# Kernel tuning notes

Measured on AMD Instinct MI355X. Metric: run time of the kernel, lower is better.

The kernel has to match this reference:

```python
import jax, jax.numpy as jnp
import numpy as np


def setup_inputs() -> dict:
    key = jax.random.key(0)
    ks = jax.random.split(key, 6)
    B, H, F, X, T = 8, 32, 8, 128, 256
    z0 = jax.random.normal(ks[0], (B, H, X), jnp.float32)
    xi = jax.random.normal(ks[1], (B, F, X, T), jnp.float32)
    A = jax.random.normal(ks[2], (H, H), jnp.float32) * 0.1
    Gw = jax.random.normal(ks[3], (H, F, H), jnp.float32) * 0.1
    Wr = jax.random.normal(ks[4], (X, H, H, H), jnp.float32) * 1e-4
    Wi = jax.random.normal(ks[5], (X, H, H, H), jnp.float32) * 1e-4
    return {"z0": z0, "xi": xi, "A": A, "Gw": Gw, "Wr": Wr, "Wi": Wi}


def reference(z0, xi, A, Gw, Wr, Wi):
    # z0: (B, H, X); xi: (B, F, X, T)
    B, Hc, X = z0.shape
    T = xi.shape[-1]

    # Initial guess u(t) = z0 for all t (reconstruction of the fixed-point seed).
    u = jnp.broadcast_to(z0[..., None], (B, Hc, X, T))

    # Linear SPDE right-hand side: Fu = A u, Gu = Gw u.
    Fu = jnp.einsum('ih,bhxt->bixt', A, u)
    Gu = jnp.einsum('ifh,bhxt->bifxt', Gw, u)          # (B, H, F, X, T)
    Guxi = jnpum = None
    Guxi = jnp.einsum('bifxt,bfxt->bixt', Gu, xi)
    Hu = Fu + Guxi                                      # (B, H, X, T)

    # Spatial FFT (axis 2) + fftshift, as in the torch module.
    H_ft = jnp.fft.fftshift(jnp.fft.fft(Hu, axis=2), axes=2)    # complex64
    z0_ft = jnp.fft.fftshift(jnp.fft.fft(z0, axis=2), axes=2)   # (B, H, X)

    # Per-Fourier-mode complex-linear CDE vector field weights.
    W = (Wr + 1j * Wi).astype(jnp.complex64)            # (X, H, H, H)

    # Control path X(t): (B, X, T, H); Euler increments at the knots.
    Hp = jnp.transpose(H_ft, (0, 2, 3, 1))
    dX = Hp[:, :, 1:, :] - Hp[:, :, :-1, :]             # (B, X, T-1, H)
    z_init = jnp.transpose(z0_ft, (0, 2, 1))            # (B, X, H)

    def step(z, dx):
        # f(z)[b, x, i, c] = sum_j W[x, i, c, j] z[b, x, j]
        fz = jnp.einsum('xicj,bxj->bxic', W, z)
        z_new = z + jnp.einsum('bxic,bxc->bxi', fz, dx)  # dz = f(z) . dX
        return z_new, z_new

    _, zs = jax.lax.scan(step, z_init, jnp.moveaxis(dX, 2, 0))
    zs = jnp.concatenate([z_init[None], zs], axis=0)    # (T, B, X, H)
    z_all = jnp.transpose(zs, (1, 3, 2, 0))             # (B, H, X, T)

    u_new = jnp.fft.ifft(jnp.fft.ifftshift(z_all, axes=2), axis=2)
    return u_new.real
```

## Files before the change

kernel.cpp:

```cpp
#include <hip/hip_runtime.h>
#include <math.h>

#define Bc 8
#define Hc 32
#define Fc 8
#define Xc 128
#define Tc 256

typedef __bf16 bf16x8 __attribute__((ext_vector_type(8)));
typedef float f32x4 __attribute__((ext_vector_type(4)));

__device__ __forceinline__ int bitrev7(int x) { return (int)(__brev((unsigned)x) >> 25); }

__device__ __forceinline__ unsigned pack_bf16(float a, float b) {
    unsigned ua = __float_as_uint(a);
    unsigned ub = __float_as_uint(b);
    ua = (ua + 0x7FFFu + ((ua >> 16) & 1u)) >> 16;
    ub = (ub + 0x7FFFu + ((ub >> 16) & 1u)) & 0xFFFF0000u;
    return (ua & 0xFFFFu) | ub;
}
__device__ __forceinline__ float bf16_val(float a) {
    unsigned ua = __float_as_uint(a);
    ua = (ua + 0x7FFFu + ((ua >> 16) & 1u)) & 0xFFFF0000u;
    return __uint_as_float(ua);
}

__device__ __forceinline__ void bfly(float2& a, float2& b, float2 twv, float sign) {
    float cs = twv.x, sn = sign * twv.y;
    float2 bw = make_float2(cs * b.x - sn * b.y, cs * b.y + sn * b.x);
    float2 na = make_float2(a.x + bw.x, a.y + bw.y);
    b = make_float2(a.x - bw.x, a.y - bw.y);
    a = na;
}

#define FRS 129
template <int NTHR>
__device__ __forceinline__ void fft32x128(float2* buf, float sign) {
    __shared__ float2 tw[128];
    int tid = threadIdx.x;
    if (tid >= 1 && tid < 128) {
        int h = 1 << (31 - __builtin_clz((unsigned)tid));
        int pos = tid - h;
        float sn, cs;
        __sincosf(3.14159265358979f * (float)pos / (float)h, &sn, &cs);
        tw[tid] = make_float2(cs, sn);
    }
    __syncthreads();
    for (int grp = tid; grp < 32 * 16; grp += NTHR) {
        float2* p = buf + (grp >> 4) * FRS + (grp & 15) * 8;
        float2 v[8];
#pragma unroll
        for (int e = 0; e < 8; ++e) v[e] = p[e];
        bfly(v[0], v[1], tw[1], sign); bfly(v[2], v[3], tw[1], sign);
        bfly(v[4], v[5], tw[1], sign); bfly(v[6], v[7], tw[1], sign);
        bfly(v[0], v[2], tw[2], sign); bfly(v[1], v[3], tw[3], sign);
        bfly(v[4], v[6], tw[2], sign); bfly(v[5], v[7], tw[3], sign);
        bfly(v[0], v[4], tw[4], sign); bfly(v[1], v[5], tw[5], sign);
        bfly(v[2], v[6], tw[6], sign); bfly(v[3], v[7], tw[7], sign);
#pragma unroll
        for (int e = 0; e < 8; ++e) p[e] = v[e];
    }
    __syncthreads();
    for (int grp = tid; grp < 32 * 32; grp += NTHR) {
        int row = grp >> 5, sub = grp & 31;
        int m = sub & 7, k = sub >> 3;
        float2* p = buf + row * FRS + k * 32 + m;
        float2 v0 = p[0], v1 = p[8], v2 = p[16], v3 = p[24];
        bfly(v0, v1, tw[8 + m], sign);
        bfly(v2, v3, tw[8 + m], sign);
        bfly(v0, v2, tw[16 + m], sign);
        bfly(v1, v3, tw[16 + m + 8], sign);
        p[0] = v0; p[8] = v1; p[16] = v2; p[24] = v3;
    }
    __syncthreads();
    for (int grp = tid; grp < 32 * 32; grp += NTHR) {
        int row = grp >> 5, m2 = grp & 31;
        float2* p = buf + row * FRS + m2;
        float2 v0 = p[0], v1 = p[32], v2 = p[64], v3 = p[96];
        bfly(v0, v1, tw[32 + m2], sign);
        bfly(v2, v3, tw[32 + m2], sign);
        bfly(v0, v2, tw[64 + m2], sign);
        bfly(v1, v3, tw[64 + m2 + 32], sign);
        p[0] = v0; p[32] = v1; p[64] = v2; p[96] = v3;
    }
    __syncthreads();
}

__global__ void k_xit(const float* __restrict__ xi, float* __restrict__ xiT) {
    __shared__ float tile[32][33];
    int bid = blockIdx.x;
    int bf = bid >> 3, tt = bid & 7;
    int t0 = tt * 32;
    int tid = threadIdx.x;
    for (int xt = 0; xt < 4; ++xt) {
        int x0 = xt * 32;
        __syncthreads();
        for (int idx = tid; idx < 1024; idx += 256) {
            int xr = idx >> 5, tc = idx & 31;
            tile[xr][tc] = xi[((size_t)bf * Xc + x0 + xr) * Tc + t0 + tc];
        }
        __syncthreads();
        for (int idx = tid; idx < 1024; idx += 256) {
            int tr = idx >> 5, xc = idx & 31;
            xiT[((size_t)bf * Tc + t0 + tr) * Xc + x0 + xc] = tile[xc][tr];
        }
    }
}

__global__ void k_pre(const float* __restrict__ z0, const float* __restrict__ A,
                      const float* __restrict__ Gw, float* __restrict__ Fz,
                      float* __restrict__ Gz, float2* __restrict__ Z0ft) {
    __shared__ float z0l[Hc * Xc];
    __shared__ float2 cbuf[Hc * FRS];
    int b = blockIdx.x;
    int tid = threadIdx.x;
    for (int idx = tid; idx < Hc * Xc; idx += 256) z0l[idx] = z0[b * Hc * Xc + idx];
    __syncthreads();
    for (int idx = tid; idx < Hc * Xc; idx += 256) {
        int i = idx >> 7, x = idx & 127;
        float s = 0.f;
        for (int h = 0; h < Hc; ++h) s += A[i * Hc + h] * z0l[h * 128 + x];
        Fz[b * Hc * Xc + idx] = s;
    }
    for (int idx = tid; idx < Hc * Fc * Xc; idx += 256) {
        int i = idx >> 10, f = (idx >> 7) & 7, x = idx & 127;
        float s = 0.f;
        for (int h = 0; h < Hc; ++h) s += Gw[(i * Fc + f) * Hc + h] * z0l[h * 128 + x];
        Gz[b * Hc * Fc * Xc + idx] = s;
    }
    for (int idx = tid; idx < Hc * Xc; idx += 256) {
        int h = idx >> 7, x = idx & 127;
        cbuf[h * FRS + bitrev7(x)] = make_float2(z0l[h * 128 + x], 0.f);
    }
    fft32x128<256>(cbuf, -1.f);
    for (int idx = tid; idx < Xc * Hc; idx += 256) {
        int xs = idx >> 5, h = idx & 31;
        Z0ft[(b * Xc + xs) * Hc + h] = cbuf[h * FRS + ((xs + 64) & 127)];
    }
}

__global__ void k_spec(const float* __restrict__ xiT, const float* __restrict__ Fz,
                       const float* __restrict__ Gz, float2* __restrict__ Hft) {
    __shared__ float xil[Fc * Xc];
    __shared__ float2 cbuf[Hc * FRS];
    int bid = blockIdx.x;
    int b = bid >> 8, t = bid & 255;
    int tid = threadIdx.x;
    for (int idx = tid; idx < Fc * Xc / 4; idx += 512) {
        int f = idx >> 5, xq = (idx & 31) * 4;
        *(float4*)(xil + f * 128 + xq) =
            *(const float4*)(xiT + ((size_t)(b * Fc + f) * Tc + t) * Xc + xq);
    }
    __syncthreads();
    for (int idx = tid; idx < Hc * Xc / 4; idx += 512) {
        int i = idx >> 5, xq = (idx & 31) * 4;
        float4 hu = *(const float4*)(Fz + b * Hc * Xc + i * 128 + xq);
        const float* gzp = Gz + (b * Hc + i) * (Fc * Xc) + xq;
#pragma unroll
        for (int f = 0; f < Fc; ++f) {
            float4 gz = *(const float4*)(gzp + f * 128);
            float4 xv = *(const float4*)(&xil[f * 128 + xq]);
            hu.x += gz.x * xv.x; hu.y += gz.y * xv.y;
            hu.z += gz.z * xv.z; hu.w += gz.w * xv.w;
        }
        cbuf[i * FRS + bitrev7(xq + 0)] = make_float2(hu.x, 0.f);
        cbuf[i * FRS + bitrev7(xq + 1)] = make_float2(hu.y, 0.f);
        cbuf[i * FRS + bitrev7(xq + 2)] = make_float2(hu.z, 0.f);
        cbuf[i * FRS + bitrev7(xq + 3)] = make_float2(hu.w, 0.f);
    }
    fft32x128<512>(cbuf, -1.f);
    for (int idx = tid; idx < Xc * Hc; idx += 512) {
        int xs = idx >> 5, i = idx & 31;
        Hft[((long)(b * Xc + xs) * Tc + t) * Hc + i] = cbuf[i * FRS + ((xs + 64) & 127)];
    }
}

#define ML_DW 16448
#define B_DW  1152
#define SCAN_LDS 150016

__device__ __forceinline__ void build_B(unsigned* Bb, int w, int tt, int c,
                                        float2 hp, float2 hn, float sc) {
    float dre = (hn.x - hp.x) * sc;
    float dim = (hn.y - hp.y) * sc;
    float hre = bf16_val(dre), hmim = bf16_val(-dim), him = bf16_val(dim);
    int n0 = w * 4 + tt * 2;
    Bb[n0 * 36 + c] = pack_bf16(hre, hmim);
    Bb[(n0 + 1) * 36 + c] = pack_bf16(him, hre);
    Bb[576 + n0 * 36 + c] = pack_bf16(dre - hre, (-dim) - hmim);
    Bb[576 + (n0 + 1) * 36 + c] = pack_bf16(dim - him, dre - hre);
}

__global__ __launch_bounds__(768, 3) void k_scan(const float* __restrict__ Wr,
                                                 const float* __restrict__ Wi,
                                                 const float2* __restrict__ Hft,
                                                 const float2* __restrict__ Z0ft,
                                                 float2* __restrict__ Zall) {
    extern __shared__ unsigned char smem[];
    float* Mlf = (float*)smem;
    unsigned* Aw = (unsigned*)smem;
    unsigned* Bd = (unsigned*)(smem + 131584);
    float* zlf = (float*)(smem + 140800);
    float2* zstc = (float2*)(smem + 141824);

    int tid = threadIdx.x;
    int x = blockIdx.x >> 1, g = blockIdx.x & 1;
    int lane = tid & 63, wid = tid >> 6;
    int isProd = (wid < 8);
    int p = wid;
    int w = isProd ? (wid & 3) : (wid - 8);
    int b = g * 4 + w;

    const float* wrp = Wr + (size_t)x * 32768;
    const float* wip = Wi + (size_t)x * 32768;
    for (int idx = tid; idx < 32768; idx += 768) {
        int j = idx & 31, cc = (idx >> 5) & 31, ii = idx >> 10;
        int r = ii * 32 + j;
        int pd = r * 32 + (((cc >> 2) ^ (r & 7)) << 2) + (cc & 3);
        Aw[pd] = pack_bf16(wrp[(ii * 32 + cc) * 32 + j], wip[(ii * 32 + cc) * 32 + j]);
    }
    __syncthreads();

    size_t bx = (size_t)(b * Xc + x);
    const float2* Hrow = Hft + bx * (Tc * Hc);
    float2* Zrow = Zall + bx * (Hc * Tc);
    int jq = lane >> 5, il = lane & 31;

    uint4 af[8][2];
    float2 Hp2 = make_float2(0.f, 0.f), Hn2 = make_float2(0.f, 0.f);
    float2 zr = make_float2(0.f, 0.f);

    if (isProd) {
        int n16 = lane & 15, q = lane >> 4;
        int rbase = p * 128 + n16;
#pragma unroll
        for (int mt = 0; mt < 8; ++mt) {
            int r = rbase + mt * 16;
#pragma unroll
            for (int kf = 0; kf < 2; ++kf) {
                int cg = (kf * 4 + q) ^ (r & 7);
                af[mt][kf] = *(const uint4*)(Aw + r * 32 + cg * 4);
            }
        }
    } else {
        __builtin_amdgcn_s_setprio(1);
        zr = Z0ft[bx * Hc + il];
        if (jq == 0) {
            ((float2*)(zlf + w * 64))[il] = zr;
            zstc[w * 256 + il] = zr;
        }
        float2 ha = Hrow[jq * 32 + il];
        float2 hb = Hrow[(1 + jq) * 32 + il];
        build_B(Bd, w, jq, il, ha, hb, 1.f);
        Hp2 = Hrow[(2 + jq) * 32 + il];
        Hn2 = Hrow[(3 + jq) * 32 + il];
    }
    __syncthreads();

#pragma unroll 1
    for (int k = 0; k <= 128; ++k) {
        if (isProd) {
            if (k < 128) {
                int bk = k & 1;
                int n = lane & 15, q = lane >> 4;
                const unsigned* Bb = Bd + bk * B_DW;
                bf16x8 bh0 = __builtin_bit_cast(bf16x8, *(const uint4*)(Bb + n * 36 + q * 4));
                bf16x8 bh1 = __builtin_bit_cast(bf16x8, *(const uint4*)(Bb + n * 36 + 16 + q * 4));
                bf16x8 bl0 = __builtin_bit_cast(bf16x8, *(const uint4*)(Bb + 576 + n * 36 + q * 4));
                bf16x8 bl1 = __builtin_bit_cast(bf16x8, *(const uint4*)(Bb + 576 + n * 36 + 16 + q * 4));
                float* Mb = Mlf + bk * ML_DW;
#pragma unroll
                for (int mt = 0; mt < 8; ++mt) {
                    f32x4 acc = {0.f, 0.f, 0.f, 0.f};
                    acc = __builtin_amdgcn_mfma_f32_16x16x32_bf16(
                        __builtin_bit_cast(bf16x8, af[mt][0]), bh0, acc, 0, 0, 0);
                    acc = __builtin_amdgcn_mfma_f32_16x16x32_bf16(
                        __builtin_bit_cast(bf16x8, af[mt][1]), bh1, acc, 0, 0, 0);
                    acc = __builtin_amdgcn_mfma_f32_16x16x32_bf16(
                        __builtin_bit_cast(bf16x8, af[mt][0]), bl0, acc, 0, 0, 0);
                    acc = __builtin_amdgcn_mfma_f32_16x16x32_bf16(
                        __builtin_bit_cast(bf16x8, af[mt][1]), bl1, acc, 0, 0, 0);
                    int i = p * 4 + (mt >> 1);
                    int jgp = ((((mt & 1) * 4) + q) ^ (i & 7)) ^ ((i >> 3) & 3);
                    *(f32x4*)(Mb + n * 1028 + i * 32 + jgp * 4) = acc;
                }
            }
        } else {
            float2 HpN = Hp2, HnN = Hn2;
            if (k + 2 <= 127) {
                int kc2 = k + 2;
                HpN = Hrow[(2 * kc2 + jq) * 32 + il];
                int t2 = 2 * kc2 + 1 + jq;
                if (t2 > 255) t2 = 255;
                HnN = Hrow[t2 * 32 + il];
            }
            if (k > 0) {
                int kc = k - 1;
                int bk = kc & 1;
#pragma unroll
                for (int s = 0; s < 2; ++s) {
                    int t = 2 * kc + 1 + s;
                    if (t > 255) break;
                    const float* base = Mlf + bk * ML_DW + (w * 4 + s * 2) * 1028 + il * 32;
                    float4 mr[4], mi[4];
#pragma unroll
                    for (int gg = 0; gg < 4; ++gg) {
                        int jg = (((jq * 4 + gg) ^ (il & 7) ^ ((il >> 3) & 3)) << 2);
                        mr[gg] = *(const float4*)(base + jg);
                        mi[gg] = *(const float4*)(base + 1028 + jg);
                    }
                    const float4* zf4 = (const float4*)(zlf + w * 64);
                    float yR = 0.f, yI = 0.f;
#pragma unroll
                    for (int gg = 0; gg < 4; ++gg) {
                        float4 za = zf4[jq * 8 + gg * 2];
                        float4 zb = zf4[jq * 8 + gg * 2 + 1];
                        yR += mr[gg].x * za.x - mi[gg].x * za.y + mr[gg].y * za.z - mi[gg].y * za.w
                            + mr[gg].z * zb.x - mi[gg].z * zb.y + mr[gg].w * zb.z - mi[gg].w * zb.w;
                        yI += mr[gg].x * za.y + mi[gg].x * za.x + mr[gg].y * za.w + mi[gg].y * za.z
                            + mr[gg].z * zb.y + mi[gg].z * zb.x + mr[gg].w * zb.w + mi[gg].w * zb.z;
                    }
                    yR += __shfl_xor(yR, 32);
                    yI += __shfl_xor(yI, 32);
                    zr.x += yR;
                    zr.y += yI;
                    if (jq == 0) {
                        ((float2*)(zlf + w * 64))[il] = zr;
                        zstc[w * 256 + (t & 7) * 32 + il] = zr;
                    }
                    if ((t & 7) == 7) {
                        int t0 = t - 7;
                        int i2 = lane >> 1, tb = (lane & 1) * 4;
                        float2 v0 = zstc[w * 256 + (tb + 0) * 32 + i2];
                        float2 v1 = zstc[w * 256 + (tb + 1) * 32 + i2];
                        float2 v2 = zstc[w * 256 + (tb + 2) * 32 + i2];
                        float2 v3 = zstc[w * 256 + (tb + 3) * 32 + i2];
                        *(float4*)(Zrow + i2 * Tc + t0 + tb) = make_float4(v0.x, v0.y, v1.x, v1.y);
                        *(float4*)(Zrow + i2 * Tc + t0 + tb + 2) = make_float4(v2.x, v2.y, v3.x, v3.y);
                    }
                }
            }
            if (k < 127) {
                float sc = (2 * (k + 1) + 1 + jq <= 255) ? 1.f : 0.f;
                build_B(Bd + ((k + 1) & 1) * B_DW, w, jq, il, Hp2, Hn2, sc);
                Hp2 = HpN;
                Hn2 = HnN;
            }
        }
        __syncthreads();
    }
}

__global__ void k_post(const float2* __restrict__ Zall, float* __restrict__ out) {
    __shared__ float2 cbuf[32 * FRS];
    int bid = blockIdx.x;
    int b = bid >> 8, i = (bid >> 3) & 31, tq = bid & 7;
    int t0 = tq * 32;
    int tid = threadIdx.x;
    for (int idx = tid; idx < 128 * 16; idx += 512) {
        int k = idx >> 4, tc2 = (idx & 15) * 2;
        int xg = (k + 64) & 127;
        float4 v = *(const float4*)(Zall + ((long)(b * Xc + xg) * Hc + i) * Tc + t0 + tc2);
        int kb = bitrev7(k);
        cbuf[tc2 * FRS + kb] = make_float2(v.x, v.y);
        cbuf[(tc2 + 1) * FRS + kb] = make_float2(v.z, v.w);
    }
    fft32x128<512>(cbuf, +1.f);
    const float inv = 1.0f / 128.0f;
    for (int idx = tid; idx < 128 * 32; idx += 512) {
        int xs = idx >> 5, tc = idx & 31;
        out[((long)(b * Hc + i) * Xc + xs) * Tc + t0 + tc] = cbuf[tc * FRS + xs].x * inv;
    }
}

extern "C" void kernel_launch(void* const* d_in, const int* in_sizes, int n_in,
                              void* d_out, int out_size, void* d_ws, size_t ws_size,
                              hipStream_t stream) {
    const float* z0 = (const float*)d_in[0];
    const float* xi = (const float*)d_in[1];
    const float* A = (const float*)d_in[2];
    const float* Gw = (const float*)d_in[3];
    const float* Wr = (const float*)d_in[4];
    const float* Wi = (const float*)d_in[5];
    float* out = (float*)d_out;
    char* ws = (char*)d_ws;

    float2* Hft = (float2*)(ws);
    float2* Zall = (float2*)(ws + 67108864);
    float2* Z0ft = (float2*)(ws + 134217728);
    float* Fz = (float*)(ws + 134479872);
    float* Gz = (float*)(ws + 134610944);
    float* xiT = (float*)(ws + 67108864);

    (void)hipFuncSetAttribute((const void*)k_scan,
                              hipFuncAttributeMaxDynamicSharedMemorySize, SCAN_LDS);

    k_xit<<<Bc * Fc * 8, 256, 0, stream>>>(xi, xiT);
    k_pre<<<Bc, 256, 0, stream>>>(z0, A, Gw, Fz, Gz, Z0ft);
    k_spec<<<Bc * Tc, 512, 0, stream>>>(xiT, Fz, Gz, Hft);
    k_scan<<<Xc * 2, 768, SCAN_LDS, stream>>>(Wr, Wi, Hft, Z0ft, Zall);
    k_post<<<Bc * Hc * 8, 512, 0, stream>>>(Zall, out);
}
```

Measured before the change: 414.2 us.

## Fuse final FFT stage into output writes and pad shared FFT layout

```diff
diff --git a/kernel.cpp b/kernel.cpp
--- a/kernel.cpp
+++ b/kernel.cpp
@@ -33,30 +33,35 @@
     a = na;
 }
 
-#define FRS 129
-template <int NTHR>
-__device__ __forceinline__ void fft32x128(float2* buf, float sign) {
-    __shared__ float2 tw[128];
-    int tid = threadIdx.x;
+#define RS 144
+__device__ __forceinline__ int AIX(int e) { return e + (e >> 3); }
+__device__ __forceinline__ int TWA(int t) { return (t >> 4) * RS + (t & 15) * 9 + 8; }
+
+__device__ __forceinline__ void fft_tw_init(float2* c, int tid) {
     if (tid >= 1 && tid < 128) {
         int h = 1 << (31 - __builtin_clz((unsigned)tid));
         int pos = tid - h;
         float sn, cs;
         __sincosf(3.14159265358979f * (float)pos / (float)h, &sn, &cs);
-        tw[tid] = make_float2(cs, sn);
-    }
-    __syncthreads();
+        c[TWA(tid)] = make_float2(cs, sn);
+    }
+}
+
+template <int NTHR>
+__device__ __forceinline__ void fft_ph12(float2* c, float sign, int tid) {
+    float2 t1 = c[TWA(1)], t2 = c[TWA(2)], t3 = c[TWA(3)];
+    float2 t4 = c[TWA(4)], t5 = c[TWA(5)], t6 = c[TWA(6)], t7 = c[TWA(7)];
     for (int grp = tid; grp < 32 * 16; grp += NTHR) {
-        float2* p = buf + (grp >> 4) * FRS + (grp & 15) * 8;
+        float2* p = c + (grp >> 4) * RS + (grp & 15) * 9;
         float2 v[8];
 #pragma unroll
         for (int e = 0; e < 8; ++e) v[e] = p[e];
-        bfly(v[0], v[1], tw[1], sign); bfly(v[2], v[3], tw[1], sign);
-        bfly(v[4], v[5], tw[1], sign); bfly(v[6], v[7], tw[1], sign);
-        bfly(v[0], v[2], tw[2], sign); bfly(v[1], v[3], tw[3], sign);
-        bfly(v[4], v[6], tw[2], sign); bfly(v[5], v[7], tw[3], sign);
-        bfly(v[0], v[4], tw[4], sign); bfly(v[1], v[5], tw[5], sign);
-        bfly(v[2], v[6], tw[6], sign); bfly(v[3], v[7], tw[7], sign);
+        bfly(v[0], v[1], t1, sign); bfly(v[2], v[3], t1, sign);
+        bfly(v[4], v[5], t1, sign); bfly(v[6], v[7], t1, sign);
+        bfly(v[0], v[2], t2, sign); bfly(v[1], v[3], t3, sign);
+        bfly(v[4], v[6], t2, sign); bfly(v[5], v[7], t3, sign);
+        bfly(v[0], v[4], t4, sign); bfly(v[1], v[5], t5, sign);
+        bfly(v[2], v[6], t6, sign); bfly(v[3], v[7], t7, sign);
 #pragma unroll
         for (int e = 0; e < 8; ++e) p[e] = v[e];
     }
@@ -64,26 +69,15 @@
     for (int grp = tid; grp < 32 * 32; grp += NTHR) {
         int row = grp >> 5, sub = grp & 31;
         int m = sub & 7, k = sub >> 3;
-        float2* p = buf + row * FRS + k * 32 + m;
-        float2 v0 = p[0], v1 = p[8], v2 = p[16], v3 = p[24];
-        bfly(v0, v1, tw[8 + m], sign);
-        bfly(v2, v3, tw[8 + m], sign);
-        bfly(v0, v2, tw[16 + m], sign);
-        bfly(v1, v3, tw[16 + m + 8], sign);
-        p[0] = v0; p[8] = v1; p[16] = v2; p[24] = v3;
-    }
-    __syncthreads();
-    for (int grp = tid; grp < 32 * 32; grp += NTHR) {
-        int row = grp >> 5, m2 = grp & 31;
-        float2* p = buf + row * FRS + m2;
-        float2 v0 = p[0], v1 = p[32], v2 = p[64], v3 = p[96];
-        bfly(v0, v1, tw[32 + m2], sign);
-        bfly(v2, v3, tw[32 + m2], sign);
-        bfly(v0, v2, tw[64 + m2], sign);
-        bfly(v1, v3, tw[64 + m2 + 32], sign);
-        p[0] = v0; p[32] = v1; p[64] = v2; p[96] = v3;
-    }
-    __syncthreads();
+        float2* p = c + row * RS + 36 * k + m;
+        float2 v0 = p[0], v1 = p[9], v2 = p[18], v3 = p[27];
+        float2 ta = c[TWA(8 + m)], tb = c[TWA(16 + m)], tc_ = c[TWA(24 + m)];
+        bfly(v0, v1, ta, sign);
+        bfly(v2, v3, ta, sign);
+        bfly(v0, v2, tb, sign);
+        bfly(v1, v3, tc_, sign);
+        p[0] = v0; p[9] = v1; p[18] = v2; p[27] = v3;
+    }
 }
 
 __global__ void k_xit(const float* __restrict__ xi, float* __restrict__ xiT) {
@@ -111,10 +105,11 @@
                       const float* __restrict__ Gw, float* __restrict__ Fz,
                       float* __restrict__ Gz, float2* __restrict__ Z0ft) {
     __shared__ float z0l[Hc * Xc];
-    __shared__ float2 cbuf[Hc * FRS];
+    __shared__ float2 cbuf[Hc * RS];
     int b = blockIdx.x;
     int tid = threadIdx.x;
     for (int idx = tid; idx < Hc * Xc; idx += 256) z0l[idx] = z0[b * Hc * Xc + idx];
+    fft_tw_init(cbuf, tid);
     __syncthreads();
     for (int idx = tid; idx < Hc * Xc; idx += 256) {
         int i = idx >> 7, x = idx & 127;
@@ -130,19 +125,31 @@
     }
     for (int idx = tid; idx < Hc * Xc; idx += 256) {
         int h = idx >> 7, x = idx & 127;
-        cbuf[h * FRS + bitrev7(x)] = make_float2(z0l[h * 128 + x], 0.f);
-    }
-    fft32x128<256>(cbuf, -1.f);
-    for (int idx = tid; idx < Xc * Hc; idx += 256) {
-        int xs = idx >> 5, h = idx & 31;
-        Z0ft[(b * Xc + xs) * Hc + h] = cbuf[h * FRS + ((xs + 64) & 127)];
+        cbuf[h * RS + AIX(bitrev7(x))] = make_float2(z0l[h * 128 + x], 0.f);
+    }
+    __syncthreads();
+    fft_ph12<256>(cbuf, -1.f, tid);
+    __syncthreads();
+    for (int grp = tid; grp < 1024; grp += 256) {
+        int h = grp & 31, m2 = grp >> 5;
+        float2* p = cbuf + h * RS + AIX(m2);
+        float2 v0 = p[0], v1 = p[36], v2 = p[72], v3 = p[108];
+        float2 ta = cbuf[TWA(32 + m2)], tb = cbuf[TWA(64 + m2)], tc_ = cbuf[TWA(96 + m2)];
+        bfly(v0, v1, ta, -1.f);
+        bfly(v2, v3, ta, -1.f);
+        bfly(v0, v2, tb, -1.f);
+        bfly(v1, v3, tc_, -1.f);
+        Z0ft[(b * Xc + m2 + 64) * Hc + h] = v0;
+        Z0ft[(b * Xc + m2 + 96) * Hc + h] = v1;
+        Z0ft[(b * Xc + m2) * Hc + h] = v2;
+        Z0ft[(b * Xc + m2 + 32) * Hc + h] = v3;
     }
 }
 
 __global__ void k_spec(const float* __restrict__ xiT, const float* __restrict__ Fz,
                        const float* __restrict__ Gz, float2* __restrict__ Hft) {
     __shared__ float xil[Fc * Xc];
-    __shared__ float2 cbuf[Hc * FRS];
+    __shared__ float2 cbuf[Hc * RS];
     int bid = blockIdx.x;
     int b = bid >> 8, t = bid & 255;
     int tid = threadIdx.x;
@@ -151,6 +158,7 @@
         *(float4*)(xil + f * 128 + xq) =
             *(const float4*)(xiT + ((size_t)(b * Fc + f) * Tc + t) * Xc + xq);
     }
+    fft_tw_init(cbuf, tid);
     __syncthreads();
     for (int idx = tid; idx < Hc * Xc / 4; idx += 512) {
         int i = idx >> 5, xq = (idx & 31) * 4;
@@ -163,15 +171,27 @@
             hu.x += gz.x * xv.x; hu.y += gz.y * xv.y;
             hu.z += gz.z * xv.z; hu.w += gz.w * xv.w;
         }
-        cbuf[i * FRS + bitrev7(xq + 0)] = make_float2(hu.x, 0.f);
-        cbuf[i * FRS + bitrev7(xq + 1)] = make_float2(hu.y, 0.f);
-        cbuf[i * FRS + bitrev7(xq + 2)] = make_float2(hu.z, 0.f);
-        cbuf[i * FRS + bitrev7(xq + 3)] = make_float2(hu.w, 0.f);
-    }
-    fft32x128<512>(cbuf, -1.f);
-    for (int idx = tid; idx < Xc * Hc; idx += 512) {
-        int xs = idx >> 5, i = idx & 31;
-        Hft[((long)(b * Xc + xs) * Tc + t) * Hc + i] = cbuf[i * FRS + ((xs + 64) & 127)];
+        cbuf[i * RS + AIX(bitrev7(xq + 0))] = make_float2(hu.x, 0.f);
+        cbuf[i * RS + AIX(bitrev7(xq + 1))] = make_float2(hu.y, 0.f);
+        cbuf[i * RS + AIX(bitrev7(xq + 2))] = make_float2(hu.z, 0.f);
+        cbuf[i * RS + AIX(bitrev7(xq + 3))] = make_float2(hu.w, 0.f);
+    }
+    __syncthreads();
+    fft_ph12<512>(cbuf, -1.f, tid);
+    __syncthreads();
+    for (int grp = tid; grp < 1024; grp += 512) {
+        int i = grp & 31, m2 = grp >> 5;
+        float2* p = cbuf + i * RS + AIX(m2);
+        float2 v0 = p[0], v1 = p[36], v2 = p[72], v3 = p[108];
+        float2 ta = cbuf[TWA(32 + m2)], tb = cbuf[TWA(64 + m2)], tc_ = cbuf[TWA(96 + m2)];
+        bfly(v0, v1, ta, -1.f);
+        bfly(v2, v3, ta, -1.f);
+        bfly(v0, v2, tb, -1.f);
+        bfly(v1, v3, tc_, -1.f);
+        Hft[((long)(b * Xc + m2 + 64) * Tc + t) * Hc + i] = v0;
+        Hft[((long)(b * Xc + m2 + 96) * Tc + t) * Hc + i] = v1;
+        Hft[((long)(b * Xc + m2) * Tc + t) * Hc + i] = v2;
+        Hft[((long)(b * Xc + m2 + 32) * Tc + t) * Hc + i] = v3;
     }
 }
 
@@ -352,7 +372,7 @@
 }
 
 __global__ void k_post(const float2* __restrict__ Zall, float* __restrict__ out) {
-    __shared__ float2 cbuf[32 * FRS];
+    __shared__ float2 cbuf[32 * RS];
     int bid = blockIdx.x;
     int b = bid >> 8, i = (bid >> 3) & 31, tq = bid & 7;
     int t0 = tq * 32;
@@ -361,15 +381,29 @@
         int k = idx >> 4, tc2 = (idx & 15) * 2;
         int xg = (k + 64) & 127;
         float4 v = *(const float4*)(Zall + ((long)(b * Xc + xg) * Hc + i) * Tc + t0 + tc2);
-        int kb = bitrev7(k);
-        cbuf[tc2 * FRS + kb] = make_float2(v.x, v.y);
-        cbuf[(tc2 + 1) * FRS + kb] = make_float2(v.z, v.w);
-    }
-    fft32x128<512>(cbuf, +1.f);
+        int ka = AIX(bitrev7(k));
+        cbuf[tc2 * RS + ka] = make_float2(v.x, v.y);
+        cbuf[(tc2 + 1) * RS + ka] = make_float2(v.z, v.w);
+    }
+    fft_tw_init(cbuf, tid);
+    __syncthreads();
+    fft_ph12<512>(cbuf, +1.f, tid);
+    __syncthreads();
     const float inv = 1.0f / 128.0f;
-    for (int idx = tid; idx < 128 * 32; idx += 512) {
-        int xs = idx >> 5, tc = idx & 31;
-        out[((long)(b * Hc + i) * Xc + xs) * Tc + t0 + tc] = cbuf[tc * FRS + xs].x * inv;
+    for (int grp = tid; grp < 1024; grp += 512) {
+        int tc = grp & 31, m2 = grp >> 5;
+        float2* p = cbuf + tc * RS + AIX(m2);
+        float2 v0 = p[0], v1 = p[36], v2 = p[72], v3 = p[108];
+        float2 ta = cbuf[TWA(32 + m2)], tb = cbuf[TWA(64 + m2)], tc_ = cbuf[TWA(96 + m2)];
+        bfly(v0, v1, ta, +1.f);
+        bfly(v2, v3, ta, +1.f);
+        bfly(v0, v2, tb, +1.f);
+        bfly(v1, v3, tc_, +1.f);
+        long ob = ((long)(b * Hc + i) * Xc) * Tc + t0 + tc;
+        out[ob + (long)(m2) * Tc] = v0.x * inv;
+        out[ob + (long)(m2 + 32) * Tc] = v1.x * inv;
+        out[ob + (long)(m2 + 64) * Tc] = v2.x * inv;
+        out[ob + (long)(m2 + 96) * Tc] = v3.x * inv;
     }
 }
 
```

Result: slower. 434.6 us (+4.9%).
